# Performance work log

Measured on AMD Instinct MI355X. Metric: run time of the kernel, lower is better.

## Reference

```python
import jax, jax.numpy as jnp
import numpy as np

N, E, H, K, C, NMOD = 50000, 600000, 128, 5, 60, 12  # nodes, edges, hidden, hops, classes, 6 blocks * 2 modules


def setup_inputs() -> dict:
    key = jax.random.key(0)
    ks = iter(jax.random.split(key, 48))
    def rn(shape, scale=0.05):
        return jax.random.normal(next(ks), shape, jnp.float32) * scale
    return {
        "node_features": rn((N, 2), 1.0),
        "lap_pe": rn((N, K), 1.0),
        "edge_feat": rn((E, 4), 1.0),
        "src": jax.random.randint(next(ks), (E,), 0, N),
        "dst": jax.random.randint(next(ks), (E,), 0, N),
        "in_w": rn((2, H)), "in_b": jnp.zeros((H,), jnp.float32),
        "pos_w": rn((K, H)), "pos_b": jnp.zeros((H,), jnp.float32),
        "edge_w": rn((4, H)), "edge_b": jnp.zeros((H,), jnp.float32),
        "conv_w": rn((NMOD, 2, (K + 1) * H, H)), "conv_b": jnp.zeros((NMOD, 2, H), jnp.float32),
        "bn_g": jnp.ones((NMOD, 2, H), jnp.float32), "bn_b": jnp.zeros((NMOD, 2, H), jnp.float32),
        "ff_w": rn((NMOD, H, H)), "ff_b": jnp.zeros((NMOD, H), jnp.float32),
        "pose_w1": rn((H, H)), "pose_b1": jnp.zeros((H,), jnp.float32),
        "pose_w2": rn((H, 3)), "pose_b2": jnp.zeros((3,), jnp.float32),
        "lab_w1": rn((H, H)), "lab_b1": jnp.zeros((H,), jnp.float32),
        "lab_w2": rn((H, C)), "lab_b2": jnp.zeros((C,), jnp.float32),
    }


def _bn(x, g, b):
    # BatchNorm1d in training mode: stats over node axis
    m = x.mean(0)
    v = x.var(0)
    return (x - m) * jax.lax.rsqrt(v + 1e-5) * g + b


def reference(node_features, lap_pe, edge_feat, src, dst,
              in_w, in_b, pos_w, pos_b, edge_w, edge_b,
              conv_w, conv_b, bn_g, bn_b, ff_w, ff_b,
              pose_w1, pose_b1, pose_w2, pose_b2,
              lab_w1, lab_b1, lab_w2, lab_b2):
    seg = jax.ops.segment_sum
    # symmetric degree norm (in-degree, clamped to 1) as in DGL TAGConv
    deg = seg(jnp.ones((E,), node_features.dtype), dst, num_segments=N)
    norm = jnp.clip(deg, 1.0) ** -0.5  # [N]

    # edge feature aggregation: copy_e -> sum onto dst
    agg_e = seg(edge_feat @ edge_w + edge_b, dst, num_segments=N)  # [N,H]
    h = node_features @ in_w + in_b + lap_pe @ pos_w + pos_b + agg_e

    def tagconv(x, W, b):
        # fstack = [x, Ax, ..., A^K x] with A = D^-1/2 A D^-1/2, then single linear
        fs = [x]
        for _ in range(K):
            z = fs[-1] * norm[:, None]
            z = seg(z[src], dst, num_segments=N) * norm[:, None]
            fs.append(z)
        return jnp.concatenate(fs, axis=-1) @ W + b  # [N,H]

    for m in range(NMOD):  # 6 blocks x 2 TAGConvModules, sequential
        h_in = h
        h = jax.nn.relu(_bn(tagconv(h, conv_w[m, 0], conv_b[m, 0]), bn_g[m, 0], bn_b[m, 0]))
        h = jax.nn.relu(_bn(tagconv(h, conv_w[m, 1], conv_b[m, 1]), bn_g[m, 1], bn_b[m, 1]))
        h = h @ ff_w[m] + ff_b[m] + h_in  # dropout = identity (eval)

    pose = jax.nn.relu(h @ pose_w1 + pose_b1) @ pose_w2 + pose_b2  # [N,3]
    y = h.mean(0)  # dgl.mean_nodes (single batched graph)
    labels = jax.nn.relu(y @ lab_w1 + lab_b1) @ lab_w2 + lab_b2  # [C]
    return pose, labels
```

## Files before the change

### kernel.cpp

```cpp
#include <hip/hip_runtime.h>

#define NN 50000
#define EE 600000
#define HH 128
#define KK 5
#define CC 60
#define NMODS 12
#define MAXPE 750080
#define SC_NB 49
#define MMGRID 391

typedef _Float16 f16;
typedef __attribute__((ext_vector_type(8))) _Float16 f16x8;
typedef __attribute__((ext_vector_type(4))) _Float16 f16x4;
typedef __attribute__((ext_vector_type(16))) float f32x16;
typedef __attribute__((ext_vector_type(4))) int int4v;
typedef __attribute__((ext_vector_type(4))) float f32x4;

#define ZSL ((size_t)NN * 128)

#define GLOBAL_AS __attribute__((address_space(1)))
#define LDS_AS __attribute__((address_space(3)))


__global__ void k_deg(const int* __restrict__ dst, int* __restrict__ deg) {
    int i = blockIdx.x * 256 + threadIdx.x;
    if (i < EE) atomicAdd(&deg[dst[i]], 1);
}

__global__ __launch_bounds__(256) void k_scan1(const int* __restrict__ deg,
                                               int* __restrict__ rs, int* __restrict__ bsum) {
    __shared__ int sm[256];
    int t = threadIdx.x;
    int base = blockIdx.x * 1024 + t * 4;
    int d[4];
#pragma unroll
    for (int j = 0; j < 4; j++) {
        int i = base + j;
        d[j] = (i < NN) ? ((deg[i] + 3) & ~3) : 0;
    }
    int sum = d[0] + d[1] + d[2] + d[3];
    sm[t] = sum;
    __syncthreads();
    for (int off = 1; off < 256; off <<= 1) {
        int v = (t >= off) ? sm[t - off] : 0;
        __syncthreads();
        sm[t] += v;
        __syncthreads();
    }
    int excl = sm[t] - sum;
    int run = excl;
#pragma unroll
    for (int j = 0; j < 4; j++) {
        int i = base + j;
        if (i < NN) rs[i] = run;
        run += d[j];
    }
    if (t == 255) bsum[blockIdx.x] = sm[t];
}

__global__ __launch_bounds__(64) void k_scan2(const int* __restrict__ bsum, int* __restrict__ binc) {
    int l = threadIdx.x;
    int v = (l < SC_NB) ? bsum[l] : 0;
#pragma unroll
    for (int off = 1; off < 64; off <<= 1) {
        int tv = __shfl_up(v, off, 64);
        if (l >= off) v += tv;
    }
    binc[l] = v;
}

__global__ __launch_bounds__(256) void k_scan3(const int* __restrict__ binc, int* __restrict__ rs) {
    int i = blockIdx.x * 256 + threadIdx.x;
    if (i < NN) {
        int b = i >> 10;
        if (b > 0) rs[i] += binc[b - 1];
    } else if (i == NN) {
        rs[NN] = binc[SC_NB - 1];
    }
}

__global__ void k_norm(const int* __restrict__ deg, float* __restrict__ norm) {
    int i = blockIdx.x * 256 + threadIdx.x;
    if (i < NN) {
        int d = deg[i];
        float fd = (float)(d < 1 ? 1 : d);
        norm[i] = 1.0f / sqrtf(fd);
    }
}

__global__ void k_fill(const int* __restrict__ src, const int* __restrict__ dst,
                       const int* __restrict__ rs, const float* __restrict__ norm,
                       int* __restrict__ cursor,
                       int* __restrict__ csrc, float* __restrict__ ew, int* __restrict__ ceid) {
    int i = blockIdx.x * 256 + threadIdx.x;
    if (i >= EE) return;
    int d = dst[i];
    int slot = atomicAdd(&cursor[d], 1);
    int p = rs[d] + slot;
    int s = src[i];
    csrc[p] = s;
    ew[p] = norm[s];
    ceid[p] = i;
}


__global__ void k_cvtw(const float* __restrict__ conv_w, const float* __restrict__ ff_w,
                       const float* __restrict__ pose_w1,
                       f16* __restrict__ wc, f16* __restrict__ wf, f16* __restrict__ wp) {
    int i = blockIdx.x * 256 + threadIdx.x;
    const int NCW = 24 * 128 * 768;
    const int NFW = 12 * 128 * 128;
    const int NPW = 128 * 128;
    if (i < NCW) {
        int mat = i / (128 * 768); int rem = i - mat * (128 * 768);
        int col = rem / 768; int k = rem - col * 768;
        wc[i] = (f16)conv_w[(size_t)mat * 768 * 128 + (size_t)k * 128 + col];
    } else if (i < NCW + NFW) {
        int j = i - NCW;
        int mat = j / (128 * 128); int rem = j - mat * (128 * 128);
        int col = rem / 128; int k = rem - col * 128;
        wf[j] = (f16)ff_w[(size_t)mat * 128 * 128 + k * 128 + col];
    } else if (i < NCW + NFW + NPW) {
        int j = i - NCW - NFW;
        int col = j / 128; int k = j - col * 128;
        wp[j] = (f16)pose_w1[k * 128 + col];
    }
}


__global__ __launch_bounds__(128) void k_h0(
    const float* __restrict__ nf, const float* __restrict__ pe, const float* __restrict__ ef,
    const int* __restrict__ rs, const int* __restrict__ ceid, const float* __restrict__ ew,
    const int* __restrict__ deg,
    const float* __restrict__ in_w, const float* __restrict__ in_b,
    const float* __restrict__ pos_w, const float* __restrict__ pos_b,
    const float* __restrict__ edge_w, const float* __restrict__ edge_b,
    float* __restrict__ h, f16* __restrict__ zc) {
    int n = blockIdx.x;
    int f = threadIdx.x;
    float v = in_b[f] + pos_b[f];
    v += nf[n * 2 + 0] * in_w[f] + nf[n * 2 + 1] * in_w[HH + f];
#pragma unroll
    for (int k = 0; k < KK; k++) v += pe[n * KK + k] * pos_w[k * HH + f];
    float e0 = edge_w[f], e1 = edge_w[HH + f], e2 = edge_w[2 * HH + f], e3 = edge_w[3 * HH + f];
    int s = rs[n], e = rs[n + 1];
    v += (float)deg[n] * edge_b[f];
    for (int i = s; i < e; i++) {
        if (ew[i] == 0.f) continue;
        int eid = ceid[i];
        float4 x = ((const float4*)ef)[eid];
        v += x.x * e0 + x.y * e1 + x.z * e2 + x.w * e3;
    }
    h[(size_t)n * HH + f] = v;
    zc[(size_t)n * 128 + f] = (f16)v;
}


__global__ __launch_bounds__(256) void k_prop16(
    const f16* __restrict__ zin, f16* __restrict__ zout,
    const float* __restrict__ norm, const int* __restrict__ rs,
    const int* __restrict__ csrc, const float* __restrict__ ew) {
    int tid = threadIdx.x;
    int n = blockIdx.x * 16 + (tid >> 4);
    if (n >= NN) return;
    int c = (tid & 15) * 8;
    int s = rs[n], e = rs[n + 1];
    const f16* zp = zin + c;
    float acc[8] = {0.f, 0.f, 0.f, 0.f, 0.f, 0.f, 0.f, 0.f};
    for (int i = s; i < e; i += 4) {
        int4v id4 = __builtin_nontemporal_load((const int4v*)(csrc + i));
        f32x4 w4 = __builtin_nontemporal_load((const f32x4*)(ew + i));
        f16x8 v0 = *(const f16x8*)(zp + (size_t)id4.x * 128);
        f16x8 v1 = *(const f16x8*)(zp + (size_t)id4.y * 128);
        f16x8 v2 = *(const f16x8*)(zp + (size_t)id4.z * 128);
        f16x8 v3 = *(const f16x8*)(zp + (size_t)id4.w * 128);
#pragma unroll
        for (int j = 0; j < 8; j++)
            acc[j] += (float)v0[j] * w4.x + (float)v1[j] * w4.y +
                      (float)v2[j] * w4.z + (float)v3[j] * w4.w;
    }
    float nw = norm[n];
    f16x8 o;
#pragma unroll
    for (int j = 0; j < 8; j++) o[j] = (f16)(acc[j] * nw);
    *(f16x8*)(zout + (size_t)n * 128 + c) = o;
}


template <int KT, int BIAS, int RESID, int RELU, int WRZ, int STATS, int YHF>
__global__ __launch_bounds__(256) void k_mm(
    const f16* __restrict__ A, const f16* __restrict__ Wt,
    const float* __restrict__ bias, const float* __restrict__ Rsd,
    float* __restrict__ Y, f16* __restrict__ Yh,
    f16* __restrict__ Zout, float* __restrict__ part) {
    __shared__ char smem[65536];
    char* As = smem;
    char* Bs = smem + 32768;
    int tid = threadIdx.x;
    int lane = tid & 63;
    int w = tid >> 6, wm = w >> 1, wn = w & 1;
    int n0 = blockIdx.x * 128;
    f32x16 acc[2][2] = {};
    for (int k0 = 0; k0 < KT; k0 += 128) {
        __syncthreads();
        const f16* Asl = A + (size_t)(k0 >> 7) * ZSL;
#pragma unroll
        for (int i = 0; i < 8; i++) {
            int p = (i * 256 + tid) * 16;
            int o = p ^ (((p >> 8) & 15) << 4);
            int r = o >> 8, ce = (o & 255) >> 1;
            int row = n0 + r; if (row >= NN) row = 0;
            const f16* ga = Asl + (size_t)row * 128 + ce;
            char* lba = As + i * 4096 + w * 1024;
            __builtin_amdgcn_global_load_lds((const GLOBAL_AS void*)ga, (LDS_AS void*)lba, 16, 0, 0);
            const f16* gb = Wt + (size_t)r * KT + k0 + ce;
            char* lbb = Bs + i * 4096 + w * 1024;
            __builtin_amdgcn_global_load_lds((const GLOBAL_AS void*)gb, (LDS_AS void*)lbb, 16, 0, 0);
        }
        asm volatile("s_waitcnt vmcnt(0)" ::: "memory");
        __syncthreads();
#pragma unroll
        for (int s = 0; s < 8; s++) {
            int koff = s * 32 + (lane >> 5) * 16;
            f16x8 a[2], b[2];
#pragma unroll
            for (int m = 0; m < 2; m++) {
                int rl = wm * 64 + m * 32 + (lane & 31);
                int oa = (rl * 256 + koff) ^ ((rl & 15) << 4);
                a[m] = *(const f16x8*)(As + oa);
                int cl = wn * 64 + m * 32 + (lane & 31);
                int ob = (cl * 256 + koff) ^ ((cl & 15) << 4);
                b[m] = *(const f16x8*)(Bs + ob);
            }
#pragma unroll
            for (int m = 0; m < 2; m++)
#pragma unroll
                for (int nb = 0; nb < 2; nb++)
                    acc[m][nb] = __builtin_amdgcn_mfma_f32_32x32x16_f16(a[m], b[nb], acc[m][nb], 0, 0, 0);
        }
    }
    float ssum[2] = {0.f, 0.f}, sqq[2] = {0.f, 0.f};
#pragma unroll
    for (int m = 0; m < 2; m++) {
        int rb = n0 + wm * 64 + m * 32 + 4 * (lane >> 5);
#pragma unroll
        for (int nb = 0; nb < 2; nb++) {
            int col = wn * 64 + nb * 32 + (lane & 31);
            float bv = 0.f;
            if (BIAS) bv = bias[col];
#pragma unroll
            for (int r = 0; r < 16; r++) {
                int row = rb + (r & 3) + 8 * (r >> 2);
                if (row >= NN) continue;
                float v = acc[m][nb][r] + bv;
                if (RESID) v += Rsd[(size_t)row * HH + col];
                if (RELU) v = fmaxf(v, 0.f);
                if (STATS) { ssum[nb] += v; sqq[nb] += v * v; }
                if (YHF) Yh[(size_t)row * HH + col] = (f16)v;
                else Y[(size_t)row * HH + col] = v;
                if (WRZ) Zout[(size_t)row * 128 + col] = (f16)v;
            }
        }
    }
    if (STATS) {
        __syncthreads();
        float* red = (float*)smem;
        int slot = wm * 2 + (lane >> 5);
        int colb = wn * 64 + (lane & 31);
        red[slot * 256 + colb] = ssum[0];
        red[slot * 256 + colb + 32] = ssum[1];
        red[slot * 256 + 128 + colb] = sqq[0];
        red[slot * 256 + 128 + colb + 32] = sqq[1];
        __syncthreads();
        float t = red[tid] + red[256 + tid] + red[512 + tid] + red[768 + tid];
        part[blockIdx.x * 256 + tid] = t;
    }
}


__global__ __launch_bounds__(128) void k_bnfin(const float* __restrict__ part,
                                               const float* __restrict__ g, const float* __restrict__ b,
                                               float* __restrict__ sc, float* __restrict__ sh) {
    int f = threadIdx.x;
    float s = 0.f, q = 0.f;
    for (int bi = 0; bi < MMGRID; bi++) {
        s += part[bi * 256 + f];
        q += part[bi * 256 + 128 + f];
    }
    float mean = s / (float)NN;
    float var = q / (float)NN - mean * mean;
    float scale = g[f] / sqrtf(var + 1e-5f);
    sc[f] = scale;
    sh[f] = b[f] - mean * scale;
}


__global__ __launch_bounds__(256) void k_bnapply(const f16* __restrict__ Yh,
                                                 const float* __restrict__ sc, const float* __restrict__ sh,
                                                 f16* __restrict__ zc) {
    int idx = blockIdx.x * 256 + threadIdx.x;
    if (idx >= NN * 16) return;
    f16x8 v = ((const f16x8*)Yh)[idx];
    int c = (idx & 15) * 8;
    f16x8 o;
#pragma unroll
    for (int j = 0; j < 8; j++) {
        float a = sc[c + j], b = sh[c + j];
        o[j] = (f16)fmaxf((float)v[j] * a + b, 0.f);
    }
    ((f16x8*)zc)[idx] = o;
}


__global__ __launch_bounds__(128) void k_pose2(const float* __restrict__ T,
                                               const float* __restrict__ W2, const float* __restrict__ b2,
                                               float* __restrict__ out) {
    int tid = threadIdx.x;
    int n = blockIdx.x * 4 + (tid >> 5);
    int c = tid & 31;
    float4 tv = ((const float4*)T)[(size_t)n * 32 + c];
    float p0 = 0.f, p1 = 0.f, p2 = 0.f;
#pragma unroll
    for (int i = 0; i < 4; i++) {
        float t = (i == 0) ? tv.x : (i == 1) ? tv.y : (i == 2) ? tv.z : tv.w;
        int k = c * 4 + i;
        p0 += t * W2[k * 3 + 0];
        p1 += t * W2[k * 3 + 1];
        p2 += t * W2[k * 3 + 2];
    }
#pragma unroll
    for (int off = 16; off > 0; off >>= 1) {
        p0 += __shfl_down(p0, off, 32);
        p1 += __shfl_down(p1, off, 32);
        p2 += __shfl_down(p2, off, 32);
    }
    if (c == 0) {
        out[(size_t)n * 3 + 0] = p0 + b2[0];
        out[(size_t)n * 3 + 1] = p1 + b2[1];
        out[(size_t)n * 3 + 2] = p2 + b2[2];
    }
}

__global__ __launch_bounds__(256) void k_meanpart(const float* __restrict__ Y, float* __restrict__ part) {
    int tid = threadIdx.x;
    float s = 0.f;
    for (int n = blockIdx.x * 2 + (tid >> 7); n < NN; n += 512) {
        s += Y[(size_t)n * HH + (tid & 127)];
    }
    __shared__ float sh[256];
    sh[tid] = s;
    __syncthreads();
    if (tid < 128) part[blockIdx.x * 128 + tid] = sh[tid] + sh[tid + 128];
}

__global__ __launch_bounds__(128) void k_labels(const float* __restrict__ part,
                                                const float* __restrict__ w1, const float* __restrict__ b1,
                                                const float* __restrict__ w2, const float* __restrict__ b2,
                                                float* __restrict__ out) {
    __shared__ float ym[128];
    __shared__ float t2[128];
    int f = threadIdx.x;
    float s = 0.f;
    for (int bi = 0; bi < 256; bi++) s += part[bi * 128 + f];
    ym[f] = s / (float)NN;
    __syncthreads();
    float a = b1[f];
    for (int k = 0; k < 128; k++) a += ym[k] * w1[k * 128 + f];
    t2[f] = fmaxf(a, 0.f);
    __syncthreads();
    if (f < CC) {
        float a2 = b2[f];
        for (int k = 0; k < 128; k++) a2 += t2[k] * w2[k * CC + f];
        out[(size_t)NN * 3 + f] = a2;
    }
}


static inline size_t align256(size_t x) { return (x + 255) & ~(size_t)255; }

extern "C" void kernel_launch(void* const* d_in, const int* in_sizes, int n_in,
                              void* d_out, int out_size, void* d_ws, size_t ws_size,
                              hipStream_t stream) {
    const float* nf = (const float*)d_in[0];
    const float* pe = (const float*)d_in[1];
    const float* ef = (const float*)d_in[2];
    const int* src = (const int*)d_in[3];
    const int* dst = (const int*)d_in[4];
    const float* in_w = (const float*)d_in[5];
    const float* in_b = (const float*)d_in[6];
    const float* pos_w = (const float*)d_in[7];
    const float* pos_b = (const float*)d_in[8];
    const float* edge_w = (const float*)d_in[9];
    const float* edge_b = (const float*)d_in[10];
    const float* conv_w = (const float*)d_in[11];
    const float* bn_g = (const float*)d_in[13];
    const float* bn_b = (const float*)d_in[14];
    const float* ff_w = (const float*)d_in[15];
    const float* ff_b = (const float*)d_in[16];
    const float* pose_w1 = (const float*)d_in[17];
    const float* pose_b1 = (const float*)d_in[18];
    const float* pose_w2 = (const float*)d_in[19];
    const float* pose_b2 = (const float*)d_in[20];
    const float* lab_w1 = (const float*)d_in[21];
    const float* lab_b1 = (const float*)d_in[22];
    const float* lab_w2 = (const float*)d_in[23];
    const float* lab_b2 = (const float*)d_in[24];
    float* out = (float*)d_out;

    char* wsp = (char*)d_ws;
    size_t off = 0;
    auto alloc = [&](size_t bytes) -> void* {
        void* p = wsp + off;
        off += align256(bytes);
        return p;
    };
    float* norm = (float*)alloc((size_t)NN * 4);
    int* deg = (int*)alloc((size_t)NN * 4);
    int* rs = (int*)alloc((size_t)(NN + 1) * 4);
    int* cursor = (int*)alloc((size_t)NN * 4);
    int* csrc = (int*)alloc((size_t)MAXPE * 4);
    float* ew = (float*)alloc((size_t)MAXPE * 4);
    int* ceid = (int*)alloc((size_t)MAXPE * 4);
    int* bsum = (int*)alloc(64 * 4);
    int* binc = (int*)alloc(64 * 4);
    float* hin = (float*)alloc((size_t)NN * HH * 4);
    float* ybuf = (float*)alloc((size_t)NN * HH * 4);
    f16* yh = (f16*)alloc((size_t)NN * HH * 2);
    f16* zcat = (f16*)alloc((size_t)6 * ZSL * 2);
    f16* wc = (f16*)alloc((size_t)24 * 128 * 768 * 2);
    f16* wf = (f16*)alloc((size_t)12 * 128 * 128 * 2);
    f16* wp = (f16*)alloc((size_t)128 * 128 * 2);
    float* part = (float*)alloc((size_t)MMGRID * 256 * 4);
    float* mpart = (float*)alloc(256 * 128 * 4);
    float* bnsc = (float*)alloc(128 * 4);
    float* bnsh = (float*)alloc(128 * 4);
    (void)ws_size; (void)in_sizes; (void)n_in; (void)out_size;

    hipMemsetAsync(deg, 0, (size_t)NN * 4, stream);
    hipMemsetAsync(cursor, 0, (size_t)NN * 4, stream);
    hipMemsetAsync(csrc, 0, (size_t)MAXPE * 4, stream);
    hipMemsetAsync(ew, 0, (size_t)MAXPE * 4, stream);
    int egrid = (EE + 255) / 256;
    k_deg<<<egrid, 256, 0, stream>>>(dst, deg);
    k_scan1<<<SC_NB, 256, 0, stream>>>(deg, rs, bsum);
    k_scan2<<<1, 64, 0, stream>>>(bsum, binc);
    k_scan3<<<(NN + 256) / 256, 256, 0, stream>>>(binc, rs);
    k_norm<<<(NN + 255) / 256, 256, 0, stream>>>(deg, norm);
    k_fill<<<egrid, 256, 0, stream>>>(src, dst, rs, norm, cursor, csrc, ew, ceid);

    const int NCVT = 24 * 128 * 768 + 12 * 128 * 128 + 128 * 128;
    k_cvtw<<<(NCVT + 255) / 256, 256, 0, stream>>>(conv_w, ff_w, pose_w1, wc, wf, wp);

    k_h0<<<NN, 128, 0, stream>>>(nf, pe, ef, rs, ceid, ew, deg, in_w, in_b, pos_w, pos_b,
                                 edge_w, edge_b, hin, zcat);

    const int pgrid = (NN + 15) / 16;
    const int agrid = (NN * 16 + 255) / 256;

    for (int m = 0; m < NMODS; m++) {
        for (int s = 0; s < 2; s++) {
            const f16* Wb = wc + (size_t)(m * 2 + s) * 128 * 768;
            for (int k = 1; k <= KK; k++) {
                k_prop16<<<pgrid, 256, 0, stream>>>(zcat + (size_t)(k - 1) * ZSL,
                                                    zcat + (size_t)k * ZSL,
                                                    norm, rs, csrc, ew);
            }
            k_mm<768, 0, 0, 0, 0, 1, 1><<<MMGRID, 256, 0, stream>>>(zcat, Wb, nullptr, nullptr,
                                                                    nullptr, yh, nullptr, part);
            k_bnfin<<<1, 128, 0, stream>>>(part, bn_g + (size_t)(m * 2 + s) * HH,
                                           bn_b + (size_t)(m * 2 + s) * HH, bnsc, bnsh);
            k_bnapply<<<agrid, 256, 0, stream>>>(yh, bnsc, bnsh, zcat);
        }
        k_mm<128, 1, 1, 0, 1, 0, 0><<<MMGRID, 256, 0, stream>>>(zcat, wf + (size_t)m * 128 * 128,
                                                                ff_b + (size_t)m * HH, hin,
                                                                hin, nullptr, zcat, nullptr);
    }

    k_mm<128, 1, 0, 1, 0, 0, 0><<<MMGRID, 256, 0, stream>>>(zcat, wp, pose_b1, nullptr,
                                                            ybuf, nullptr, nullptr, nullptr);
    k_pose2<<<NN / 4, 128, 0, stream>>>(ybuf, pose_w2, pose_b2, out);

    k_meanpart<<<256, 256, 0, stream>>>(hin, mpart);
    k_labels<<<1, 128, 0, stream>>>(mpart, lab_w1, lab_b1, lab_w2, lab_b2, out);
}
```

Before: 4.957 ms.

## Partition CSR by source range and pack index with fp16 weight

Builds a second CSR keyed by (source quarter, destination), padding each segment to an even length. Each neighbour entry is stored as a 32-bit word holding a 16-bit source id and an fp16 edge weight. The propagation kernel handles two nodes per 16-lane group and walks the four source partitions in order, so gathers within each pass touch a narrower range of the feature table, which should improve L2 locality and halve index/weight traffic. In exchange it adds preprocessing kernels, runs more short inner loops per node, and rounds edge weights to fp16.

```diff
diff --git a/kernel.cpp b/kernel.cpp
--- a/kernel.cpp
+++ b/kernel.cpp
@@ -9,6 +9,11 @@
 #define MAXPE 750080
 #define SC_NB 49
 #define MMGRID 391
+#define RQ 12500
+#define M4 (4 * NN)
+#define SC4_NB 196
+#define MAXPE4 802816
+#define NB4 1563
 
 typedef _Float16 f16;
 typedef __attribute__((ext_vector_type(8))) _Float16 f16x8;
@@ -92,16 +97,98 @@
 __global__ void k_fill(const int* __restrict__ src, const int* __restrict__ dst,
                        const int* __restrict__ rs, const float* __restrict__ norm,
                        int* __restrict__ cursor,
-                       int* __restrict__ csrc, float* __restrict__ ew, int* __restrict__ ceid) {
+                       float* __restrict__ ew, int* __restrict__ ceid) {
     int i = blockIdx.x * 256 + threadIdx.x;
     if (i >= EE) return;
     int d = dst[i];
     int slot = atomicAdd(&cursor[d], 1);
     int p = rs[d] + slot;
     int s = src[i];
-    csrc[p] = s;
     ew[p] = norm[s];
     ceid[p] = i;
+}
+
+
+__global__ void k_deg4(const int* __restrict__ src, const int* __restrict__ dst,
+                       int* __restrict__ deg4) {
+    int i = blockIdx.x * 256 + threadIdx.x;
+    if (i < EE) {
+        int p = src[i] / RQ;
+        atomicAdd(&deg4[p * NN + dst[i]], 1);
+    }
+}
+
+__global__ __launch_bounds__(256) void k_scan1b(const int* __restrict__ deg4,
+                                                int* __restrict__ rs4, int* __restrict__ bsum) {
+    __shared__ int sm[256];
+    int t = threadIdx.x;
+    int base = blockIdx.x * 1024 + t * 4;
+    int d[4];
+#pragma unroll
+    for (int j = 0; j < 4; j++) {
+        int i = base + j;
+        d[j] = (i < M4) ? ((deg4[i] + 1) & ~1) : 0;
+    }
+    int sum = d[0] + d[1] + d[2] + d[3];
+    sm[t] = sum;
+    __syncthreads();
+    for (int off = 1; off < 256; off <<= 1) {
+        int v = (t >= off) ? sm[t - off] : 0;
+        __syncthreads();
+        sm[t] += v;
+        __syncthreads();
+    }
+    int excl = sm[t] - sum;
+    int run = excl;
+#pragma unroll
+    for (int j = 0; j < 4; j++) {
+        int i = base + j;
+        if (i < M4) rs4[i] = run;
+        run += d[j];
+    }
+    if (t == 255) bsum[blockIdx.x] = sm[t];
+}
+
+__global__ __launch_bounds__(256) void k_scan2b(const int* __restrict__ bsum, int* __restrict__ binc) {
+    __shared__ int sm[256];
+    int t = threadIdx.x;
+    int v = (t < SC4_NB) ? bsum[t] : 0;
+    sm[t] = v;
+    __syncthreads();
+    for (int off = 1; off < 256; off <<= 1) {
+        int tv = (t >= off) ? sm[t - off] : 0;
+        __syncthreads();
+        sm[t] += tv;
+        __syncthreads();
+    }
+    binc[t] = sm[t];
+}
+
+__global__ __launch_bounds__(256) void k_scan3b(const int* __restrict__ binc, int* __restrict__ rs4) {
+    int i = blockIdx.x * 256 + threadIdx.x;
+    if (i < M4) {
+        int b = i >> 10;
+        if (b > 0) rs4[i] += binc[b - 1];
+    } else if (i == M4) {
+        rs4[M4] = binc[SC4_NB - 1];
+    }
+}
+
+__global__ void k_fill4(const int* __restrict__ src, const int* __restrict__ dst,
+                        const int* __restrict__ rs4, const float* __restrict__ norm,
+                        int* __restrict__ cursor4, unsigned int* __restrict__ cpk4) {
+    int i = blockIdx.x * 256 + threadIdx.x;
+    if (i >= EE) return;
+    int s = src[i];
+    int p = s / RQ;
+    int d = dst[i];
+    int key = p * NN + d;
+    int slot = atomicAdd(&cursor4[key], 1);
+    int pos = rs4[key] + slot;
+    f16 w = (f16)norm[s];
+    unsigned short wb;
+    __builtin_memcpy(&wb, &w, 2);
+    cpk4[pos] = (unsigned int)s | ((unsigned int)wb << 16);
 }
 
 
@@ -157,34 +244,55 @@
 }
 
 
-__global__ __launch_bounds__(256) void k_prop16(
+__global__ __launch_bounds__(256) void k_prop4(
     const f16* __restrict__ zin, f16* __restrict__ zout,
-    const float* __restrict__ norm, const int* __restrict__ rs,
-    const int* __restrict__ csrc, const float* __restrict__ ew) {
+    const float* __restrict__ norm, const int* __restrict__ rs4,
+    const unsigned int* __restrict__ cpk4) {
     int tid = threadIdx.x;
-    int n = blockIdx.x * 16 + (tid >> 4);
-    if (n >= NN) return;
+    int g = tid >> 4;
     int c = (tid & 15) * 8;
-    int s = rs[n], e = rs[n + 1];
+    int n0 = (blockIdx.x * 16 + g) * 2;
     const f16* zp = zin + c;
-    float acc[8] = {0.f, 0.f, 0.f, 0.f, 0.f, 0.f, 0.f, 0.f};
-    for (int i = s; i < e; i += 4) {
-        int4v id4 = __builtin_nontemporal_load((const int4v*)(csrc + i));
-        f32x4 w4 = __builtin_nontemporal_load((const f32x4*)(ew + i));
-        f16x8 v0 = *(const f16x8*)(zp + (size_t)id4.x * 128);
-        f16x8 v1 = *(const f16x8*)(zp + (size_t)id4.y * 128);
-        f16x8 v2 = *(const f16x8*)(zp + (size_t)id4.z * 128);
-        f16x8 v3 = *(const f16x8*)(zp + (size_t)id4.w * 128);
-#pragma unroll
-        for (int j = 0; j < 8; j++)
-            acc[j] += (float)v0[j] * w4.x + (float)v1[j] * w4.y +
-                      (float)v2[j] * w4.z + (float)v3[j] * w4.w;
-    }
-    float nw = norm[n];
-    f16x8 o;
-#pragma unroll
-    for (int j = 0; j < 8; j++) o[j] = (f16)(acc[j] * nw);
-    *(f16x8*)(zout + (size_t)n * 128 + c) = o;
+    float acc0[8] = {0.f, 0.f, 0.f, 0.f, 0.f, 0.f, 0.f, 0.f};
+    float acc1[8] = {0.f, 0.f, 0.f, 0.f, 0.f, 0.f, 0.f, 0.f};
+#pragma unroll
+    for (int p = 0; p < 4; ++p) {
+#pragma unroll
+        for (int nd = 0; nd < 2; ++nd) {
+            int n = n0 + nd;
+            if (n >= NN) continue;
+            float* acc = nd ? acc1 : acc0;
+            int base = p * NN + n;
+            int i0 = rs4[base], i1 = rs4[base + 1];
+#pragma unroll 2
+            for (int i = i0; i < i1; i += 2) {
+                unsigned int pk0 = cpk4[i], pk1 = cpk4[i + 1];
+                int s0 = pk0 & 0xFFFF, s1 = pk1 & 0xFFFF;
+                unsigned short b0 = (unsigned short)(pk0 >> 16);
+                unsigned short b1 = (unsigned short)(pk1 >> 16);
+                f16 h0, h1;
+                __builtin_memcpy(&h0, &b0, 2);
+                __builtin_memcpy(&h1, &b1, 2);
+                float w0 = (float)h0, w1 = (float)h1;
+                f16x8 v0 = *(const f16x8*)(zp + (size_t)s0 * 128);
+                f16x8 v1 = *(const f16x8*)(zp + (size_t)s1 * 128);
+#pragma unroll
+                for (int j = 0; j < 8; j++)
+                    acc[j] += (float)v0[j] * w0 + (float)v1[j] * w1;
+            }
+        }
+    }
+#pragma unroll
+    for (int nd = 0; nd < 2; ++nd) {
+        int n = n0 + nd;
+        if (n >= NN) continue;
+        float* acc = nd ? acc1 : acc0;
+        float nw = norm[n];
+        f16x8 o;
+#pragma unroll
+        for (int j = 0; j < 8; j++) o[j] = (f16)(acc[j] * nw);
+        *(f16x8*)(zout + (size_t)n * 128 + c) = o;
+    }
 }
 
 
@@ -294,7 +402,6 @@
     sc[f] = scale;
     sh[f] = b[f] - mean * scale;
 }
-
 
 __global__ __launch_bounds__(256) void k_bnapply(const f16* __restrict__ Yh,
                                                  const float* __restrict__ sc, const float* __restrict__ sh,
@@ -419,11 +526,16 @@
     int* deg = (int*)alloc((size_t)NN * 4);
     int* rs = (int*)alloc((size_t)(NN + 1) * 4);
     int* cursor = (int*)alloc((size_t)NN * 4);
-    int* csrc = (int*)alloc((size_t)MAXPE * 4);
     float* ew = (float*)alloc((size_t)MAXPE * 4);
     int* ceid = (int*)alloc((size_t)MAXPE * 4);
     int* bsum = (int*)alloc(64 * 4);
     int* binc = (int*)alloc(64 * 4);
+    int* deg4 = (int*)alloc((size_t)M4 * 4);
+    int* rs4 = (int*)alloc((size_t)(M4 + 1) * 4);
+    int* cursor4 = (int*)alloc((size_t)M4 * 4);
+    unsigned int* cpk4 = (unsigned int*)alloc((size_t)MAXPE4 * 4);
+    int* bsum4 = (int*)alloc(256 * 4);
+    int* binc4 = (int*)alloc(256 * 4);
     float* hin = (float*)alloc((size_t)NN * HH * 4);
     float* ybuf = (float*)alloc((size_t)NN * HH * 4);
     f16* yh = (f16*)alloc((size_t)NN * HH * 2);
@@ -439,7 +551,6 @@
 
     hipMemsetAsync(deg, 0, (size_t)NN * 4, stream);
     hipMemsetAsync(cursor, 0, (size_t)NN * 4, stream);
-    hipMemsetAsync(csrc, 0, (size_t)MAXPE * 4, stream);
     hipMemsetAsync(ew, 0, (size_t)MAXPE * 4, stream);
     int egrid = (EE + 255) / 256;
     k_deg<<<egrid, 256, 0, stream>>>(dst, deg);
@@ -447,7 +558,16 @@
     k_scan2<<<1, 64, 0, stream>>>(bsum, binc);
     k_scan3<<<(NN + 256) / 256, 256, 0, stream>>>(binc, rs);
     k_norm<<<(NN + 255) / 256, 256, 0, stream>>>(deg, norm);
-    k_fill<<<egrid, 256, 0, stream>>>(src, dst, rs, norm, cursor, csrc, ew, ceid);
+    k_fill<<<egrid, 256, 0, stream>>>(src, dst, rs, norm, cursor, ew, ceid);
+
+    hipMemsetAsync(deg4, 0, (size_t)M4 * 4, stream);
+    hipMemsetAsync(cursor4, 0, (size_t)M4 * 4, stream);
+    hipMemsetAsync(cpk4, 0, (size_t)MAXPE4 * 4, stream);
+    k_deg4<<<egrid, 256, 0, stream>>>(src, dst, deg4);
+    k_scan1b<<<SC4_NB, 256, 0, stream>>>(deg4, rs4, bsum4);
+    k_scan2b<<<1, 256, 0, stream>>>(bsum4, binc4);
+    k_scan3b<<<(M4 + 256) / 256, 256, 0, stream>>>(binc4, rs4);
+    k_fill4<<<egrid, 256, 0, stream>>>(src, dst, rs4, norm, cursor4, cpk4);
 
     const int NCVT = 24 * 128 * 768 + 12 * 128 * 128 + 128 * 128;
     k_cvtw<<<(NCVT + 255) / 256, 256, 0, stream>>>(conv_w, ff_w, pose_w1, wc, wf, wp);
@@ -455,16 +575,15 @@
     k_h0<<<NN, 128, 0, stream>>>(nf, pe, ef, rs, ceid, ew, deg, in_w, in_b, pos_w, pos_b,
                                  edge_w, edge_b, hin, zcat);
 
-    const int pgrid = (NN + 15) / 16;
     const int agrid = (NN * 16 + 255) / 256;
 
     for (int m = 0; m < NMODS; m++) {
         for (int s = 0; s < 2; s++) {
             const f16* Wb = wc + (size_t)(m * 2 + s) * 128 * 768;
             for (int k = 1; k <= KK; k++) {
-                k_prop16<<<pgrid, 256, 0, stream>>>(zcat + (size_t)(k - 1) * ZSL,
-                                                    zcat + (size_t)k * ZSL,
-                                                    norm, rs, csrc, ew);
+                k_prop4<<<NB4, 256, 0, stream>>>(zcat + (size_t)(k - 1) * ZSL,
+                                                 zcat + (size_t)k * ZSL,
+                                                 norm, rs4, cpk4);
             }
             k_mm<768, 0, 0, 0, 0, 1, 1><<<MMGRID, 256, 0, stream>>>(zcat, Wb, nullptr, nullptr,
                                                                     nullptr, yh, nullptr, part);
```

Measured after the change: 4.971 ms. No clear change (+0.3%).
